# Kernel tuning notes

Hardware: AMD Instinct MI355X
Metric: run time of the kernel (lower is better)

## Reference

```python
import jax, jax.numpy as jnp
import numpy as np

B, T, F, H = 1024, 512, 40, 50


def setup_inputs() -> dict:
    key = jax.random.key(0)
    ks = jax.random.split(key, 9)
    s = 0.1
    return {
        "x": jax.random.normal(ks[0], (B, T, F), dtype=jnp.float32),
        "W_ih": jax.random.normal(ks[1], (4 * H, F), dtype=jnp.float32) * s,
        "W_hh": jax.random.normal(ks[2], (4 * H, H), dtype=jnp.float32) * s,
        "b_ih": jax.random.normal(ks[3], (4 * H,), dtype=jnp.float32) * s,
        "b_hh": jax.random.normal(ks[4], (4 * H,), dtype=jnp.float32) * s,
        "W1": jax.random.normal(ks[5], (10, H), dtype=jnp.float32) * s,
        "b1": jax.random.normal(ks[6], (10,), dtype=jnp.float32) * s,
        "W2": jax.random.normal(ks[7], (1, 10), dtype=jnp.float32) * s,
        "b2": jax.random.normal(ks[8], (1,), dtype=jnp.float32) * s,
    }


def reference(x, W_ih, W_hh, b_ih, b_hh, W1, b1, W2, b2):
    b, t, f = x.shape
    h = W_hh.shape[1]
    # Precompute input projections for all timesteps: [T, B, 4H]
    xg = jnp.einsum("btf,gf->tbg", x, W_ih) + (b_ih + b_hh)

    h0 = jnp.zeros((b, h), dtype=x.dtype)
    c0 = jnp.zeros((b, h), dtype=x.dtype).at[:, 0].set(1.0)

    def step(carry, xg_t):
        hx, cx = carry
        gates = xg_t + hx @ W_hh.T  # [B, 4H]
        i, fg, g, o = jnp.split(gates, 4, axis=-1)  # PyTorch gate order i,f,g,o
        i = jax.nn.sigmoid(i)
        fg = jax.nn.sigmoid(fg)
        g = jnp.tanh(g)
        o = jax.nn.sigmoid(o)
        cx = fg * cx + i * g
        hx = o * jnp.tanh(cx)
        return (hx, cx), None

    (hx, _), _ = jax.lax.scan(step, (h0, c0), xg)
    head = jax.nn.relu(hx @ W1.T + b1) @ W2.T + b2  # [B, 1]
    return head + x[:, -1, 0:1]
```

## Files before the change

kernel.cpp:

```cpp
#include <hip/hip_runtime.h>


constexpr int kT   = 512;
constexpr int kF   = 40;
constexpr int kH   = 50;
constexpr int kMB  = 2;
constexpr int kRowS = 104;
constexpr int kGRow = 208;

typedef __attribute__((ext_vector_type(8))) short bf16x8;
typedef __attribute__((ext_vector_type(4))) float f32x4;

__device__ __forceinline__ unsigned short f2bf(float f) {
    union { float f; unsigned u; } v; v.f = f;
    return (unsigned short)((v.u + 0x7FFFu + ((v.u >> 16) & 1u)) >> 16);
}
__device__ __forceinline__ float fast_sigmoid(float v) {
    return __builtin_amdgcn_rcpf(1.f + __expf(-v));
}
__device__ __forceinline__ float fast_tanh(float v) {
    return 1.f - 2.f * __builtin_amdgcn_rcpf(__expf(2.f * v) + 1.f);
}

__global__ __launch_bounds__(256, 2)
void lstm_mfma_rawbar(
    const float* __restrict__ x,
    const float* __restrict__ W_ih,
    const float* __restrict__ W_hh,
    const float* __restrict__ b_ih,
    const float* __restrict__ b_hh,
    const float* __restrict__ W1,
    const float* __restrict__ b1,
    const float* __restrict__ W2,
    const float* __restrict__ b2,
    float* __restrict__ out)
{
    const int tid  = threadIdx.x;
    const int lane = tid & 63;
    const int wave = tid >> 6;
    const int bb   = blockIdx.x;
    const int m16  = lane & 15;
    const int q    = lane >> 4;

    __shared__ short sh_comb[2][16][kRowS];
    __shared__ float sh_g[kMB][kGRow];
    __shared__ float sh_hf[kMB][kH + 2];
    __shared__ float sh_head[kMB][10];

    const int t0 = (wave == 3) ? 9 : wave * 3;
    const int NT = (wave == 3) ? 4 : 3;

    { int* z = (int*)sh_comb; for (int i = tid; i < 1664; i += 256) z[i] = 0; }

    bf16x8 wa[4][3];
    float  bias[4][4];
    const int uA = m16 >> 2, gA = m16 & 3;
#pragma unroll
    for (int i = 0; i < 4; ++i) {
        const int tl = t0 + i;
        const int unitA = 4 * tl + uA;
        const bool live = (i < NT) && (unitA < kH);
        const int orow = live ? (unitA + 50 * gA) : 0;
#pragma unroll
        for (int kk = 0; kk < 3; ++kk) {
            bf16x8 v;
#pragma unroll
            for (int j = 0; j < 8; ++j) {
                const int k = kk * 32 + q * 8 + j;
                float wv = 0.f;
                if (live) {
                    if (k < kF)           wv = W_ih[orow * kF + k];
                    else if (k < kF + kH) wv = W_hh[orow * kH + (k - kF)];
                }
                v[j] = (short)f2bf(wv);
            }
            wa[i][kk] = v;
        }
        const int uD = 4 * tl + q;
#pragma unroll
        for (int r = 0; r < 4; ++r)
            bias[i][r] = (i < NT && uD < kH)
                       ? (b_ih[uD + 50 * r] + b_hh[uD + 50 * r]) : 0.f;
    }

    const bool pw = (tid < kMB * kH);
    const int  pm = pw ? (tid / kH) : 0;
    const int  pu = pw ? (tid % kH) : 0;
    float c     = (pw && pu == 0) ? 1.f : 0.f;
    float lasth = 0.f;

    const bool xs = (tid >= 128 && tid < 128 + kMB * 20);
    const int  xi = xs ? (tid - 128) : 0;
    const int  xm = xi / 20, xd = xi % 20;
    const float* xrow = x + ((size_t)(bb * kMB + xm) * kT) * kF + 2 * xd;

    float2 pa = {0.f, 0.f}, pb = {0.f, 0.f};
    __syncthreads();
    if (xs) {
        float2 v0 = *(const float2*)xrow;
        unsigned pk = (unsigned)f2bf(v0.x) | ((unsigned)f2bf(v0.y) << 16);
        *(unsigned*)&sh_comb[0][xm][2 * xd] = pk;
        pa = *(const float2*)(xrow + (size_t)1 * kF);
        pb = *(const float2*)(xrow + (size_t)2 * kF);
    }
    __syncthreads();

    auto step = [&](int t, int CUR, float2& pf) {
        const short* rowp = &sh_comb[CUR][m16][0];
        bf16x8 bv0 = *(const bf16x8*)(rowp +      q * 8);
        bf16x8 bv1 = *(const bf16x8*)(rowp + 32 + q * 8);
        bf16x8 bv2 = *(const bf16x8*)(rowp + 64 + q * 8);
#pragma unroll
        for (int i = 0; i < 4; ++i) {
            if (i < NT) {
                f32x4 d;
                d[0] = bias[i][0]; d[1] = bias[i][1];
                d[2] = bias[i][2]; d[3] = bias[i][3];
                d = __builtin_amdgcn_mfma_f32_16x16x32_bf16(wa[i][0], bv0, d, 0, 0, 0);
                d = __builtin_amdgcn_mfma_f32_16x16x32_bf16(wa[i][1], bv1, d, 0, 0, 0);
                d = __builtin_amdgcn_mfma_f32_16x16x32_bf16(wa[i][2], bv2, d, 0, 0, 0);
                if (m16 < kMB)
                    *(f32x4*)&sh_g[m16][16 * (t0 + i) + 4 * q] = d;
            }
        }
        asm volatile("s_waitcnt lgkmcnt(0)\n\ts_barrier" ::: "memory");

        short* nbuf = &sh_comb[CUR ^ 1][0][0];
        if (pw) {
            f32x4 g = *(const f32x4*)&sh_g[pm][4 * pu];
            float i_s = fast_sigmoid(g[0]);
            float f_s = fast_sigmoid(g[1]);
            float g_t = fast_tanh   (g[2]);
            float o_s = fast_sigmoid(g[3]);
            c = fmaf(f_s, c, i_s * g_t);
            lasth = o_s * fast_tanh(c);
            if (t + 1 < kT)
                nbuf[pm * kRowS + kF + pu] = (short)f2bf(lasth);
        } else if (xs) {
            if (t + 1 < kT) {
                unsigned pk = (unsigned)f2bf(pf.x) | ((unsigned)f2bf(pf.y) << 16);
                *(unsigned*)&nbuf[xm * kRowS + 2 * xd] = pk;
            }
            if (t + 3 < kT)
                pf = *(const float2*)(xrow + (size_t)(t + 3) * kF);
        }
        asm volatile("s_waitcnt lgkmcnt(0)\n\ts_barrier" ::: "memory");
    };

    for (int t = 0; t < kT; t += 2) {
        step(t,     0, pa);
        step(t + 1, 1, pb);
    }

    if (pw) sh_hf[pm][pu] = lasth;
    __syncthreads();
    if (tid < kMB * 10) {
        const int m = tid / 10, j = tid % 10;
        float acc = b1[j];
#pragma unroll
        for (int k = 0; k < kH; ++k) acc = fmaf(sh_hf[m][k], W1[j * kH + k], acc);
        sh_head[m][j] = fmaxf(acc, 0.f);
    }
    __syncthreads();
    if (tid < kMB) {
        float acc = b2[0];
#pragma unroll
        for (int j2 = 0; j2 < 10; ++j2) acc = fmaf(sh_head[tid][j2], W2[j2], acc);
        const int bidx = bb * kMB + tid;
        out[bidx] = acc + x[((size_t)bidx * kT + (kT - 1)) * kF];
    }
}

extern "C" void kernel_launch(void* const* d_in, const int* in_sizes, int n_in,
                              void* d_out, int out_size, void* d_ws, size_t ws_size,
                              hipStream_t stream) {
    const float* x    = (const float*)d_in[0];
    const float* W_ih = (const float*)d_in[1];
    const float* W_hh = (const float*)d_in[2];
    const float* b_ih = (const float*)d_in[3];
    const float* b_hh = (const float*)d_in[4];
    const float* W1   = (const float*)d_in[5];
    const float* b1   = (const float*)d_in[6];
    const float* W2   = (const float*)d_in[7];
    const float* b2   = (const float*)d_in[8];
    float* out = (float*)d_out;

    lstm_mfma_rawbar<<<dim3(1024 / kMB), dim3(256), 0, stream>>>(
        x, W_ih, W_hh, b_ih, b_hh, W1, b1, W2, b2, out);
}
```

Before: 358.5 us.

## Split input projection off the recurrent path and precompute it one step ahead

The K dimension is split into separate h and x operands in separate shared buffers. The x-projection MFMAs for step t+1 are issued during the elementwise phase of step t, so the critical path between barriers holds only two MFMAs per tile instead of three. This adds a fourth weight chunk per tile in registers, more MFMAs in total (4 instead of 3), and a deeper x prefetch with more shared memory.

```diff
diff --git a/kernel.cpp b/kernel.cpp
--- a/kernel.cpp
+++ b/kernel.cpp
@@ -5,7 +5,7 @@
 constexpr int kF   = 40;
 constexpr int kH   = 50;
 constexpr int kMB  = 2;
-constexpr int kRowS = 104;
+constexpr int kPR  = 72;
 constexpr int kGRow = 208;
 
 typedef __attribute__((ext_vector_type(8))) short bf16x8;
@@ -23,7 +23,7 @@
 }
 
 __global__ __launch_bounds__(256, 2)
-void lstm_mfma_rawbar(
+void lstm_mfma_pipe(
     const float* __restrict__ x,
     const float* __restrict__ W_ih,
     const float* __restrict__ W_hh,
@@ -42,7 +42,7 @@
     const int m16  = lane & 15;
     const int q    = lane >> 4;
 
-    __shared__ short sh_comb[2][16][kRowS];
+    __shared__ short shP[4][16][kPR];
     __shared__ float sh_g[kMB][kGRow];
     __shared__ float sh_hf[kMB][kH + 2];
     __shared__ float sh_head[kMB][10];
@@ -50,10 +50,10 @@
     const int t0 = (wave == 3) ? 9 : wave * 3;
     const int NT = (wave == 3) ? 4 : 3;
 
-    { int* z = (int*)sh_comb; for (int i = tid; i < 1664; i += 256) z[i] = 0; }
-
-    bf16x8 wa[4][3];
-    float  bias[4][4];
+    { int* z = (int*)shP; for (int i = tid; i < 2304; i += 256) z[i] = 0; }
+
+    bf16x8 wa[4][4];
+    f32x4  bias4[4];
     const int uA = m16 >> 2, gA = m16 & 3;
 #pragma unroll
     for (int i = 0; i < 4; ++i) {
@@ -62,25 +62,29 @@
         const bool live = (i < NT) && (unitA < kH);
         const int orow = live ? (unitA + 50 * gA) : 0;
 #pragma unroll
-        for (int kk = 0; kk < 3; ++kk) {
+        for (int c = 0; c < 4; ++c) {
             bf16x8 v;
 #pragma unroll
             for (int j = 0; j < 8; ++j) {
-                const int k = kk * 32 + q * 8 + j;
                 float wv = 0.f;
                 if (live) {
-                    if (k < kF)           wv = W_ih[orow * kF + k];
-                    else if (k < kF + kH) wv = W_hh[orow * kH + (k - kF)];
+                    if (c < 2) {
+                        const int k = 32 * c + q * 8 + j;
+                        if (k < kH) wv = W_hh[orow * kH + k];
+                    } else {
+                        const int xc = 32 * (c - 2) + q * 8 + j;
+                        if (xc < kF) wv = W_ih[orow * kF + xc];
+                    }
                 }
                 v[j] = (short)f2bf(wv);
             }
-            wa[i][kk] = v;
+            wa[i][c] = v;
         }
         const int uD = 4 * tl + q;
 #pragma unroll
         for (int r = 0; r < 4; ++r)
-            bias[i][r] = (i < NT && uD < kH)
-                       ? (b_ih[uD + 50 * r] + b_hh[uD + 50 * r]) : 0.f;
+            bias4[i][r] = (i < NT && uD < kH)
+                        ? (b_ih[uD + 50 * r] + b_hh[uD + 50 * r]) : 0.f;
     }
 
     const bool pw = (tid < kMB * kH);
@@ -98,34 +102,48 @@
     __syncthreads();
     if (xs) {
         float2 v0 = *(const float2*)xrow;
-        unsigned pk = (unsigned)f2bf(v0.x) | ((unsigned)f2bf(v0.y) << 16);
-        *(unsigned*)&sh_comb[0][xm][2 * xd] = pk;
-        pa = *(const float2*)(xrow + (size_t)1 * kF);
-        pb = *(const float2*)(xrow + (size_t)2 * kF);
-    }
-    __syncthreads();
-
-    auto step = [&](int t, int CUR, float2& pf) {
-        const short* rowp = &sh_comb[CUR][m16][0];
-        bf16x8 bv0 = *(const bf16x8*)(rowp +      q * 8);
-        bf16x8 bv1 = *(const bf16x8*)(rowp + 32 + q * 8);
-        bf16x8 bv2 = *(const bf16x8*)(rowp + 64 + q * 8);
+        unsigned p0 = (unsigned)f2bf(v0.x) | ((unsigned)f2bf(v0.y) << 16);
+        *(unsigned*)&shP[2][xm][2 * xd] = p0;
+        float2 v1 = *(const float2*)(xrow + (size_t)1 * kF);
+        unsigned p1 = (unsigned)f2bf(v1.x) | ((unsigned)f2bf(v1.y) << 16);
+        *(unsigned*)&shP[3][xm][2 * xd] = p1;
+        pa = *(const float2*)(xrow + (size_t)2 * kF);
+        pb = *(const float2*)(xrow + (size_t)3 * kF);
+    }
+    __syncthreads();
+
+    f32x4 dp[4];
+    {
+        const short* xp = &shP[2][m16][0];
+        bf16x8 xv0 = *(const bf16x8*)(xp + q * 8);
+        bf16x8 xv1 = *(const bf16x8*)(xp + 32 + q * 8);
 #pragma unroll
         for (int i = 0; i < 4; ++i) {
             if (i < NT) {
-                f32x4 d;
-                d[0] = bias[i][0]; d[1] = bias[i][1];
-                d[2] = bias[i][2]; d[3] = bias[i][3];
-                d = __builtin_amdgcn_mfma_f32_16x16x32_bf16(wa[i][0], bv0, d, 0, 0, 0);
-                d = __builtin_amdgcn_mfma_f32_16x16x32_bf16(wa[i][1], bv1, d, 0, 0, 0);
-                d = __builtin_amdgcn_mfma_f32_16x16x32_bf16(wa[i][2], bv2, d, 0, 0, 0);
+                f32x4 d = bias4[i];
+                d = __builtin_amdgcn_mfma_f32_16x16x32_bf16(wa[i][2], xv0, d, 0, 0, 0);
+                d = __builtin_amdgcn_mfma_f32_16x16x32_bf16(wa[i][3], xv1, d, 0, 0, 0);
+                dp[i] = d;
+            }
+        }
+    }
+
+    auto step = [&](int t, int CUR, float2& pf) {
+        const short* hp = &shP[CUR][m16][0];
+        bf16x8 h0 = *(const bf16x8*)(hp + q * 8);
+        bf16x8 h1 = *(const bf16x8*)(hp + 32 + q * 8);
+#pragma unroll
+        for (int i = 0; i < 4; ++i) {
+            if (i < NT) {
+                f32x4 d = dp[i];
+                d = __builtin_amdgcn_mfma_f32_16x16x32_bf16(wa[i][0], h0, d, 0, 0, 0);
+                d = __builtin_amdgcn_mfma_f32_16x16x32_bf16(wa[i][1], h1, d, 0, 0, 0);
                 if (m16 < kMB)
                     *(f32x4*)&sh_g[m16][16 * (t0 + i) + 4 * q] = d;
             }
         }
         asm volatile("s_waitcnt lgkmcnt(0)\n\ts_barrier" ::: "memory");
 
-        short* nbuf = &sh_comb[CUR ^ 1][0][0];
         if (pw) {
             f32x4 g = *(const f32x4*)&sh_g[pm][4 * pu];
             float i_s = fast_sigmoid(g[0]);
@@ -135,14 +153,28 @@
             c = fmaf(f_s, c, i_s * g_t);
             lasth = o_s * fast_tanh(c);
             if (t + 1 < kT)
-                nbuf[pm * kRowS + kF + pu] = (short)f2bf(lasth);
+                shP[CUR ^ 1][pm][pu] = (short)f2bf(lasth);
         } else if (xs) {
-            if (t + 1 < kT) {
+            if (t + 2 < kT) {
                 unsigned pk = (unsigned)f2bf(pf.x) | ((unsigned)f2bf(pf.y) << 16);
-                *(unsigned*)&nbuf[xm * kRowS + 2 * xd] = pk;
-            }
-            if (t + 3 < kT)
-                pf = *(const float2*)(xrow + (size_t)(t + 3) * kF);
+                *(unsigned*)&shP[2 + CUR][xm][2 * xd] = pk;
+            }
+            if (t + 4 < kT)
+                pf = *(const float2*)(xrow + (size_t)(t + 4) * kF);
+        }
+        if (t + 1 < kT) {
+            const short* xp = &shP[2 + (CUR ^ 1)][m16][0];
+            bf16x8 xv0 = *(const bf16x8*)(xp + q * 8);
+            bf16x8 xv1 = *(const bf16x8*)(xp + 32 + q * 8);
+#pragma unroll
+            for (int i = 0; i < 4; ++i) {
+                if (i < NT) {
+                    f32x4 d = bias4[i];
+                    d = __builtin_amdgcn_mfma_f32_16x16x32_bf16(wa[i][2], xv0, d, 0, 0, 0);
+                    d = __builtin_amdgcn_mfma_f32_16x16x32_bf16(wa[i][3], xv1, d, 0, 0, 0);
+                    dp[i] = d;
+                }
+            }
         }
         asm volatile("s_waitcnt lgkmcnt(0)\n\ts_barrier" ::: "memory");
     };
@@ -185,6 +217,6 @@
     const float* b2   = (const float*)d_in[8];
     float* out = (float*)d_out;
 
-    lstm_mfma_rawbar<<<dim3(1024 / kMB), dim3(256), 0, stream>>>(
+    lstm_mfma_pipe<<<dim3(1024 / kMB), dim3(256), 0, stream>>>(
         x, W_ih, W_hh, b_ih, b_hh, W1, b1, W2, b2, out);
 }
```

Result: slower. 385.5 us (+7.5%).
